# Performance work log

Measured on AMD Instinct MI355X. Metric: run time of the kernel, lower is better.

## Reference

```python
import jax, jax.numpy as jnp
import numpy as np
from jax import lax

NUM_ITERATIONS = 3
KAPPA = 0.05
DT = 0.25
EPS = 1e-8

# Sobel kernels, normalized by 8, matching the torch buffers. OIHW layout.
_sx = np.array([[-1, 0, 1], [-2, 0, 2], [-1, 0, 1]], dtype=np.float32) / 8.0
_sy = np.array([[-1, -2, -1], [0, 0, 0], [1, 2, 1]], dtype=np.float32) / 8.0
SOBEL_XY = jnp.asarray(np.stack([_sx, _sy])[:, None])  # (2,1,3,3)

_DN = ('NCHW', 'OIHW', 'NCHW')


def _conv(x, w, groups=1):
    return lax.conv_general_dilated(
        x, w, window_strides=(1, 1), padding='SAME',
        dimension_numbers=_DN, feature_group_count=groups)


def setup_inputs() -> dict:
    key = jax.random.key(0)
    image = jax.random.uniform(key, (16, 1, 1024, 1024), dtype=jnp.float32)
    return {"image": image}


def reference(image) -> jnp.ndarray:
    result = image
    for _ in range(NUM_ITERATIONS):
        # (N,2,H,W): ch0 = grad_x, ch1 = grad_y
        grads = _conv(result, SOBEL_XY)
        grad_mag = jnp.sqrt(jnp.sum(grads * grads, axis=1, keepdims=True) + EPS)
        # Perona-Malik g2 conduction: 1 / (1 + (|grad|/kappa)^2)
        c = 1.0 / (1.0 + (grad_mag / KAPPA) ** 2)
        flux = c * grads
        # grouped conv: d/dx on flux_x, d/dy on flux_y, then sum -> divergence
        div_xy = _conv(flux, SOBEL_XY, groups=2)
        divergence = jnp.sum(div_xy, axis=1, keepdims=True)
        result = result + DT * divergence
    return result
```

## Files before the change

### kernel.cpp

```cpp
#include <hip/hip_runtime.h>

#define IMG 1024
#define BH 16
#define ROWW 1032
#define PAD 4

__global__ __launch_bounds__(256, 4) void pm_sweep(const float* __restrict__ in,
                                                   float* __restrict__ out) {
    __shared__ __align__(16) float lds[9 * ROWW];
    float* const sIN = lds;
    float* const sFX = lds + 3 * ROWW;
    float* const sFY = lds + 6 * ROWW;

    const int tid = threadIdx.x;
    const int y0  = blockIdx.x * BH;
    const size_t base = (size_t)blockIdx.y * IMG * IMG;
    const float* I = in + base;
    float*       O = out + base;
    const int c0 = tid << 2;
    const int di = PAD + c0;

    float r0[4] = {0,0,0,0}, r1[4] = {0,0,0,0}, r2[4] = {0,0,0,0};
    float fx1[4] = {0,0,0,0}, fx2[4] = {0,0,0,0};
    float fy1[4] = {0,0,0,0}, fy2[4] = {0,0,0,0};
    float4 Lp;

    {
        const int row = y0 - 2;
        if (row >= 0) Lp = *(const float4*)(I + ((size_t)row << 10) + c0);
        else          Lp = make_float4(0.f, 0.f, 0.f, 0.f);
    }
    if (tid < 72) {
        const int r = tid >> 3, j = tid & 7;
        lds[r * ROWW + ((j < 4) ? j : (1024 + j))] = 0.f;
    }
    __syncthreads();

    int slI = 0;
    for (int k = 0; k < BH + 4; ++k) {
        const int yld = y0 - 2 + k;

        *(float4*)(sIN + slI * ROWW + di) = Lp;
        #pragma unroll
        for (int j = 0; j < 4; ++j) { r2[j] = r1[j]; r1[j] = r0[j]; }
        r0[0] = Lp.x; r0[1] = Lp.y; r0[2] = Lp.z; r0[3] = Lp.w;

        if (k <= BH + 2) {
            const int row = yld + 1;
            if (row >= 0 && row < IMG)
                Lp = *(const float4*)(I + ((size_t)row << 10) + c0);
            else
                Lp = make_float4(0.f, 0.f, 0.f, 0.f);
        }
        __syncthreads();

        const int sl1 = (slI == 2) ? 0 : slI + 1;
        const int sl2 = (sl1 == 2) ? 0 : sl1 + 1;

        float fxN[4], fyN[4];
        if (k >= 2) {
            const int yf = yld - 1;
            if (yf >= 0 && yf < IMG) {
                float um[6], uc[6], up[6];
                um[0] = sIN[sl1*ROWW + di - 1]; um[5] = sIN[sl1*ROWW + di + 4];
                uc[0] = sIN[sl2*ROWW + di - 1]; uc[5] = sIN[sl2*ROWW + di + 4];
                up[0] = sIN[slI*ROWW + di - 1]; up[5] = sIN[slI*ROWW + di + 4];
                #pragma unroll
                for (int j = 0; j < 4; ++j) { um[j+1] = r2[j]; uc[j+1] = r1[j]; up[j+1] = r0[j]; }
                float s[6], d[6];
                #pragma unroll
                for (int j = 0; j < 6; ++j) {
                    s[j] = fmaf(2.f, uc[j], um[j] + up[j]);
                    d[j] = up[j] - um[j];
                }
                #pragma unroll
                for (int i = 0; i < 4; ++i) {
                    const float GX = s[i+2] - s[i];
                    const float GY = fmaf(2.f, d[i+1], d[i] + d[i+2]);
                    const float m2 = fmaf(GY, GY, GX * GX);
                    const float mag = fmaf(m2, 0.015625f, 1e-8f);
                    const float den = fmaf(mag, 400.f, 1.f);
                    const float c = __builtin_amdgcn_rcpf(den);
                    fxN[i] = c * GX;
                    fyN[i] = c * GY;
                }
            } else {
                #pragma unroll
                for (int i = 0; i < 4; ++i) { fxN[i] = 0.f; fyN[i] = 0.f; }
            }
            *(float4*)(sFX + sl2*ROWW + di) = make_float4(fxN[0], fxN[1], fxN[2], fxN[3]);
            *(float4*)(sFY + sl2*ROWW + di) = make_float4(fyN[0], fyN[1], fyN[2], fyN[3]);
        }
        __syncthreads();

        if (k >= 4) {
            const int yd = yld - 2;
            float xm[6], xc[6], xp[6], ym[6], yp[6];
            xm[0] = sFX[slI*ROWW + di - 1]; xm[5] = sFX[slI*ROWW + di + 4];
            xc[0] = sFX[sl1*ROWW + di - 1]; xc[5] = sFX[sl1*ROWW + di + 4];
            xp[0] = sFX[sl2*ROWW + di - 1]; xp[5] = sFX[sl2*ROWW + di + 4];
            ym[0] = sFY[slI*ROWW + di - 1]; ym[5] = sFY[slI*ROWW + di + 4];
            yp[0] = sFY[sl2*ROWW + di - 1]; yp[5] = sFY[sl2*ROWW + di + 4];
            #pragma unroll
            for (int j = 0; j < 4; ++j) {
                xm[j+1] = fx2[j]; xc[j+1] = fx1[j]; xp[j+1] = fxN[j];
                ym[j+1] = fy2[j];                   yp[j+1] = fyN[j];
            }
            float S2[6], D2[6];
            #pragma unroll
            for (int j = 0; j < 6; ++j) {
                S2[j] = fmaf(2.f, xc[j], xm[j] + xp[j]);
                D2[j] = yp[j] - ym[j];
            }
            float o[4];
            #pragma unroll
            for (int i = 0; i < 4; ++i) {
                const float DX = S2[i+2] - S2[i];
                const float DY = fmaf(2.f, D2[i+1], D2[i] + D2[i+2]);
                o[i] = fmaf(DX + DY, 0.00390625f, r2[i]);
            }
            *(float4*)(O + ((size_t)yd << 10) + c0) = make_float4(o[0], o[1], o[2], o[3]);
        }

        if (k >= 2) {
            #pragma unroll
            for (int j = 0; j < 4; ++j) {
                fx2[j] = fx1[j]; fx1[j] = fxN[j];
                fy2[j] = fy1[j]; fy1[j] = fyN[j];
            }
        }
        slI = (slI == 2) ? 0 : slI + 1;
    }
}

extern "C" void kernel_launch(void* const* d_in, const int* in_sizes, int n_in,
                              void* d_out, int out_size, void* d_ws, size_t ws_size,
                              hipStream_t stream) {
    const float* img = (const float*)d_in[0];
    float* out = (float*)d_out;
    float* ws  = (float*)d_ws;
    const int N = in_sizes[0] / (IMG * IMG);

    dim3 grid(IMG / BH, N);
    dim3 block(256);
    pm_sweep<<<grid, block, 0, stream>>>(img, out);
    pm_sweep<<<grid, block, 0, stream>>>(out, ws);
    pm_sweep<<<grid, block, 0, stream>>>(ws, out);
}
```

Measured before the change: 174.2 us.

## Replace LDS halo exchange with overlapping global loads and redundant flux compute

Removes the shared-memory row buffers and the two barriers per row. Each thread now loads two overlapping float4s per row to get a 2-column halo from global memory, and recomputes the flux for 6 columns instead of 4 so no neighbour exchange is needed. This trades LDS traffic and __syncthreads for doubled global load requests (mostly L1/L2 hits) and about 50% more flux arithmetic. The row loop is also fully unrolled.

```diff
diff --git a/kernel.cpp b/kernel.cpp
--- a/kernel.cpp
+++ b/kernel.cpp
@@ -1,135 +1,106 @@
 #include <hip/hip_runtime.h>
 
 #define IMG 1024
-#define BH 16
-#define ROWW 1032
-#define PAD 4
+#define BH  16
 
-__global__ __launch_bounds__(256, 4) void pm_sweep(const float* __restrict__ in,
-                                                   float* __restrict__ out) {
-    __shared__ __align__(16) float lds[9 * ROWW];
-    float* const sIN = lds;
-    float* const sFX = lds + 3 * ROWW;
-    float* const sFY = lds + 6 * ROWW;
-
+__global__ __launch_bounds__(256, 4)
+void pm_sweep(const float* __restrict__ in, float* __restrict__ out) {
     const int tid = threadIdx.x;
+    const int c0  = tid << 2;
     const int y0  = blockIdx.x * BH;
-    const size_t base = (size_t)blockIdx.y * IMG * IMG;
+    const size_t base = (size_t)blockIdx.y << 20;
     const float* I = in + base;
     float*       O = out + base;
-    const int c0 = tid << 2;
-    const int di = PAD + c0;
 
-    float r0[4] = {0,0,0,0}, r1[4] = {0,0,0,0}, r2[4] = {0,0,0,0};
-    float fx1[4] = {0,0,0,0}, fx2[4] = {0,0,0,0};
-    float fy1[4] = {0,0,0,0}, fy2[4] = {0,0,0,0};
-    float4 Lp;
+    const bool le = (c0 == 0);
+    const bool re = (c0 == IMG - 4);
+    const int aC = le ? 0 : c0 - 2;
+    const int bC = re ? IMG - 4 : c0 + 2;
 
-    {
-        const int row = y0 - 2;
-        if (row >= 0) Lp = *(const float4*)(I + ((size_t)row << 10) + c0);
-        else          Lp = make_float4(0.f, 0.f, 0.f, 0.f);
+    float r0[8], r1[8], r2[8];
+    float f1x[6], f1y[6], f2x[6], f2y[6];
+    #pragma unroll
+    for (int j = 0; j < 8; ++j) { r0[j] = 0.f; r1[j] = 0.f; r2[j] = 0.f; }
+    #pragma unroll
+    for (int j = 0; j < 6; ++j) { f1x[j] = 0.f; f1y[j] = 0.f; f2x[j] = 0.f; f2y[j] = 0.f; }
+
+    float4 A = make_float4(0.f, 0.f, 0.f, 0.f), B = A;
+    if (y0 >= 2) {
+        const size_t r = (size_t)(y0 - 2) << 10;
+        A = *(const float4*)(I + r + aC);
+        B = *(const float4*)(I + r + bC);
     }
-    if (tid < 72) {
-        const int r = tid >> 3, j = tid & 7;
-        lds[r * ROWW + ((j < 4) ? j : (1024 + j))] = 0.f;
-    }
-    __syncthreads();
 
-    int slI = 0;
+    #pragma unroll
     for (int k = 0; k < BH + 4; ++k) {
         const int yld = y0 - 2 + k;
 
-        *(float4*)(sIN + slI * ROWW + di) = Lp;
         #pragma unroll
-        for (int j = 0; j < 4; ++j) { r2[j] = r1[j]; r1[j] = r0[j]; }
-        r0[0] = Lp.x; r0[1] = Lp.y; r0[2] = Lp.z; r0[3] = Lp.w;
+        for (int j = 0; j < 8; ++j) { r2[j] = r1[j]; r1[j] = r0[j]; }
+        r0[0] = le ? 0.f : A.x;  r0[1] = le ? 0.f : A.y;
+        r0[2] = le ? A.x : A.z;  r0[3] = le ? A.y : A.w;
+        r0[4] = re ? B.z : B.x;  r0[5] = re ? B.w : B.y;
+        r0[6] = re ? 0.f : B.z;  r0[7] = re ? 0.f : B.w;
 
-        if (k <= BH + 2) {
+        if (k < BH + 3) {
             const int row = yld + 1;
-            if (row >= 0 && row < IMG)
-                Lp = *(const float4*)(I + ((size_t)row << 10) + c0);
-            else
-                Lp = make_float4(0.f, 0.f, 0.f, 0.f);
+            if (row >= 0 && row < IMG) {
+                const size_t r = (size_t)row << 10;
+                A = *(const float4*)(I + r + aC);
+                B = *(const float4*)(I + r + bC);
+            } else { A = make_float4(0.f, 0.f, 0.f, 0.f); B = A; }
         }
-        __syncthreads();
 
-        const int sl1 = (slI == 2) ? 0 : slI + 1;
-        const int sl2 = (sl1 == 2) ? 0 : sl1 + 1;
-
-        float fxN[4], fyN[4];
-        if (k >= 2) {
-            const int yf = yld - 1;
-            if (yf >= 0 && yf < IMG) {
-                float um[6], uc[6], up[6];
-                um[0] = sIN[sl1*ROWW + di - 1]; um[5] = sIN[sl1*ROWW + di + 4];
-                uc[0] = sIN[sl2*ROWW + di - 1]; uc[5] = sIN[sl2*ROWW + di + 4];
-                up[0] = sIN[slI*ROWW + di - 1]; up[5] = sIN[slI*ROWW + di + 4];
-                #pragma unroll
-                for (int j = 0; j < 4; ++j) { um[j+1] = r2[j]; uc[j+1] = r1[j]; up[j+1] = r0[j]; }
-                float s[6], d[6];
-                #pragma unroll
-                for (int j = 0; j < 6; ++j) {
-                    s[j] = fmaf(2.f, uc[j], um[j] + up[j]);
-                    d[j] = up[j] - um[j];
-                }
-                #pragma unroll
-                for (int i = 0; i < 4; ++i) {
-                    const float GX = s[i+2] - s[i];
-                    const float GY = fmaf(2.f, d[i+1], d[i] + d[i+2]);
-                    const float m2 = fmaf(GY, GY, GX * GX);
-                    const float mag = fmaf(m2, 0.015625f, 1e-8f);
-                    const float den = fmaf(mag, 400.f, 1.f);
-                    const float c = __builtin_amdgcn_rcpf(den);
-                    fxN[i] = c * GX;
-                    fyN[i] = c * GY;
-                }
-            } else {
-                #pragma unroll
-                for (int i = 0; i < 4; ++i) { fxN[i] = 0.f; fyN[i] = 0.f; }
+        float fNx[6], fNy[6];
+        const int yf = yld - 1;
+        if (yf >= 0 && yf < IMG) {
+            float s[8], d[8];
+            #pragma unroll
+            for (int j = 0; j < 8; ++j) {
+                s[j] = fmaf(2.f, r1[j], r2[j] + r0[j]);
+                d[j] = r0[j] - r2[j];
             }
-            *(float4*)(sFX + sl2*ROWW + di) = make_float4(fxN[0], fxN[1], fxN[2], fxN[3]);
-            *(float4*)(sFY + sl2*ROWW + di) = make_float4(fyN[0], fyN[1], fyN[2], fyN[3]);
+            #pragma unroll
+            for (int i = 0; i < 6; ++i) {
+                const float GX  = s[i+2] - s[i];
+                const float GY  = fmaf(2.f, d[i+1], d[i] + d[i+2]);
+                const float m2  = fmaf(GY, GY, GX * GX);
+                const float mag = fmaf(m2, 0.015625f, 1e-8f);
+                const float den = fmaf(mag, 400.f, 1.f);
+                const float c   = __builtin_amdgcn_rcpf(den);
+                fNx[i] = c * GX;
+                fNy[i] = c * GY;
+            }
+            if (le) { fNx[0] = 0.f; fNy[0] = 0.f; }
+            if (re) { fNx[5] = 0.f; fNy[5] = 0.f; }
+        } else {
+            #pragma unroll
+            for (int i = 0; i < 6; ++i) { fNx[i] = 0.f; fNy[i] = 0.f; }
         }
-        __syncthreads();
 
         if (k >= 4) {
-            const int yd = yld - 2;
-            float xm[6], xc[6], xp[6], ym[6], yp[6];
-            xm[0] = sFX[slI*ROWW + di - 1]; xm[5] = sFX[slI*ROWW + di + 4];
-            xc[0] = sFX[sl1*ROWW + di - 1]; xc[5] = sFX[sl1*ROWW + di + 4];
-            xp[0] = sFX[sl2*ROWW + di - 1]; xp[5] = sFX[sl2*ROWW + di + 4];
-            ym[0] = sFY[slI*ROWW + di - 1]; ym[5] = sFY[slI*ROWW + di + 4];
-            yp[0] = sFY[sl2*ROWW + di - 1]; yp[5] = sFY[sl2*ROWW + di + 4];
-            #pragma unroll
-            for (int j = 0; j < 4; ++j) {
-                xm[j+1] = fx2[j]; xc[j+1] = fx1[j]; xp[j+1] = fxN[j];
-                ym[j+1] = fy2[j];                   yp[j+1] = fyN[j];
-            }
-            float S2[6], D2[6];
+            float S[6], D[6];
             #pragma unroll
             for (int j = 0; j < 6; ++j) {
-                S2[j] = fmaf(2.f, xc[j], xm[j] + xp[j]);
-                D2[j] = yp[j] - ym[j];
+                S[j] = fmaf(2.f, f1x[j], f2x[j] + fNx[j]);
+                D[j] = fNy[j] - f2y[j];
             }
             float o[4];
             #pragma unroll
             for (int i = 0; i < 4; ++i) {
-                const float DX = S2[i+2] - S2[i];
-                const float DY = fmaf(2.f, D2[i+1], D2[i] + D2[i+2]);
-                o[i] = fmaf(DX + DY, 0.00390625f, r2[i]);
+                const float DX = S[i+2] - S[i];
+                const float DY = fmaf(2.f, D[i+1], D[i] + D[i+2]);
+                o[i] = fmaf(DX + DY, 0.00390625f, r2[i+2]);
             }
+            const int yd = yld - 2;
             *(float4*)(O + ((size_t)yd << 10) + c0) = make_float4(o[0], o[1], o[2], o[3]);
         }
 
-        if (k >= 2) {
-            #pragma unroll
-            for (int j = 0; j < 4; ++j) {
-                fx2[j] = fx1[j]; fx1[j] = fxN[j];
-                fy2[j] = fy1[j]; fy1[j] = fyN[j];
-            }
+        #pragma unroll
+        for (int j = 0; j < 6; ++j) {
+            f2x[j] = f1x[j]; f2y[j] = f1y[j];
+            f1x[j] = fNx[j]; f1y[j] = fNy[j];
         }
-        slI = (slI == 2) ? 0 : slI + 1;
     }
 }
 
```

After: 165.8 us. -4.8%, faster.
